# Performance work log

Measured on AMD Instinct MI355X. Metric: run time of the kernel, lower is better.

The kernel has to match this reference:

```python
import jax, jax.numpy as jnp
import numpy as np

V, C, H, L, E, D, B, T = 32000, 1024, 16, 3, 8, 1024, 8, 512
FF = 4 * C
EPS = 1e-5


def setup_inputs() -> dict:
    key = jax.random.key(0)
    ks = iter(jax.random.split(key, 32))
    def w(shape, s=0.02):
        return jax.random.normal(next(ks), shape, jnp.float32) * s
    return {
        "idx": jax.random.randint(next(ks), (B, T), 0, V),
        "tok_emb": w((V, C)),
        "ln1_g": jnp.ones((L, C)), "ln1_b": jnp.zeros((L, C)),
        "ln2_g": jnp.ones((L, C)), "ln2_b": jnp.zeros((L, C)),
        "qkv_w": w((L, C, 3 * C)), "proj_w": w((L, C, C)),
        "ff_w1": w((L, C, FF)), "ff_b1": jnp.zeros((L, FF)),
        "ff_w2": w((L, FF, C)), "ff_b2": jnp.zeros((L, C)),
        "router_w": w((C, E)),
        "exp_w1": w((E, C, D)), "exp_b1": jnp.zeros((E, D)),
        "exp_w2": w((E, D, C)), "exp_b2": jnp.zeros((E, C)),
        "lnf_g": jnp.ones((C,)), "lnf_b": jnp.zeros((C,)),
        "head_w": w((C, V)),
    }


def layernorm(x, g, b):
    m = x.mean(-1, keepdims=True)
    v = x.var(-1, keepdims=True)
    return (x - m) * jax.lax.rsqrt(v + EPS) * g + b


def rope_cos_sin(t, d):
    inv = 1.0 / (10000.0 ** (jnp.arange(0, d, 2, dtype=jnp.float32) / d))
    fr = jnp.arange(t, dtype=jnp.float32)[:, None] * inv[None, :]  # [T, d/2]
    emb = jnp.concatenate([fr, fr], -1)  # [T, d]
    return jnp.cos(emb), jnp.sin(emb)


def rot_half(x):
    x1, x2 = jnp.split(x, 2, axis=-1)
    return jnp.concatenate([-x2, x1], -1)


def attn(x, qkv_w, proj_w):
    b, t, c = x.shape
    d = c // H
    qkv = (x @ qkv_w).reshape(b, t, 3, H, d).transpose(2, 0, 3, 1, 4)  # [3,B,H,T,d]
    q, k, v = qkv[0], qkv[1], qkv[2]
    cos, sin = rope_cos_sin(t, d)
    q = q * cos + rot_half(q) * sin
    k = k * cos + rot_half(k) * sin
    s = jnp.einsum('bhqd,bhkd->bhqk', q, k) / np.float32(np.sqrt(d))
    causal = jnp.tril(jnp.ones((t, t), bool))
    s = jnp.where(causal, s, jnp.float32(-1e30))
    a = jax.nn.softmax(s, -1)
    y = jnp.einsum('bhqk,bhkd->bhqd', a, v)
    y = y.transpose(0, 2, 1, 3).reshape(b, t, c)
    return y @ proj_w


def moe(xf, router_w, exp_w1, exp_b1, exp_w2, exp_b2):
    # router softmax -> top-2 -> renormalize -> scatter into dense [N,E] mask
    probs = jax.nn.softmax(xf @ router_w, -1)
    tw, ti = jax.lax.top_k(probs, 2)
    tw = tw / tw.sum(-1, keepdims=True)
    n = xf.shape[0]
    mask = jnp.zeros((n, E), xf.dtype).at[jnp.arange(n)[:, None], ti].set(tw)
    # per-expert dense FFN over all tokens, combined with sparse weights
    h = jax.nn.gelu(jnp.einsum('nc,ecd->end', xf, exp_w1) + exp_b1[:, None, :], approximate=False)
    y = jnp.einsum('end,edc->enc', h, exp_w2) + exp_b2[:, None, :]
    return jnp.einsum('ne,enc->nc', mask, y)


def reference(idx, tok_emb, ln1_g, ln1_b, ln2_g, ln2_b, qkv_w, proj_w,
              ff_w1, ff_b1, ff_w2, ff_b2, router_w, exp_w1, exp_b1,
              exp_w2, exp_b2, lnf_g, lnf_b, head_w):
    x = tok_emb[idx]  # [B,T,C]
    for l in range(L):
        x = x + attn(layernorm(x, ln1_g[l], ln1_b[l]), qkv_w[l], proj_w[l])
        h = layernorm(x, ln2_g[l], ln2_b[l])
        x = x + (jax.nn.gelu(h @ ff_w1[l] + ff_b1[l], approximate=False) @ ff_w2[l] + ff_b2[l])
    b, t, c = x.shape
    x = moe(x.reshape(b * t, c), router_w, exp_w1, exp_b1, exp_w2, exp_b2).reshape(b, t, c)
    x = layernorm(x, lnf_g, lnf_b)
    return x @ head_w  # logits [B,T,V]
```

## Files before the change

kernel.cpp:

```cpp
#include <hip/hip_runtime.h>
#include <math.h>


#define NTOK  4096
#define CDIM  1024
#define HEADS 16
#define DHEAD 64
#define LAYERS 3
#define NEXP  8
#define DEXP  1024
#define TSEQ  512
#define FFDIM 4096
#define VOCAB 32000
#define C3    3072

typedef __attribute__((ext_vector_type(8))) short short8;
typedef __attribute__((ext_vector_type(4))) float f32x4;

__device__ __forceinline__ unsigned short f2bf(float f) {
  unsigned int u = __builtin_bit_cast(unsigned int, f);
  return (unsigned short)((u + 0x7fffu + ((u >> 16) & 1u)) >> 16);
}
__device__ __forceinline__ float bf2f(unsigned short h) {
  return __builtin_bit_cast(float, ((unsigned int)h) << 16);
}

__global__ __launch_bounds__(256) void embed_kernel(const int* __restrict__ idx,
                                                    const float* __restrict__ emb,
                                                    float* __restrict__ x) {
  int i = blockIdx.x * 256 + threadIdx.x;
  int n = i >> 8, c4 = i & 255;
  const float4* src = (const float4*)(emb + (size_t)idx[n] * CDIM);
  ((float4*)(x + (size_t)n * CDIM))[c4] = src[c4];
}

__global__ void rope_table_kernel(float* __restrict__ ct, float* __restrict__ st) {
  int t = blockIdx.x, p = threadIdx.x;
  float inv = powf(10000.0f, -(float)p / 32.0f);
  float ang = (float)t * inv;
  ct[t * 32 + p] = cosf(ang);
  st[t * 32 + p] = sinf(ang);
}

__global__ __launch_bounds__(256) void qkv_prep_kernel(
    const float* __restrict__ qkv, const float* __restrict__ ct,
    const float* __restrict__ st,
    unsigned short* __restrict__ Qh, unsigned short* __restrict__ Qm,
    unsigned short* __restrict__ Ql,
    unsigned short* __restrict__ Kh, unsigned short* __restrict__ Km,
    unsigned short* __restrict__ Kl,
    unsigned short* __restrict__ Vth, unsigned short* __restrict__ Vtm,
    unsigned short* __restrict__ Vtl) {
  __shared__ unsigned short sVh[64 * 64], sVm[64 * 64], sVl[64 * 64];
  const int tid = threadIdx.x;
  const int tt0 = blockIdx.x * 64, h = blockIdx.y, b = blockIdx.z;
  const int bh = b * HEADS + h;
#pragma unroll
  for (int u = 0; u < 8; u++) {
    int pidx = tid + u * 256;
    int tl = pidx >> 5, p = pidx & 31;
    int t = tt0 + tl;
    size_t nb = ((size_t)(b * TSEQ + t)) * C3 + h * DHEAD;
    float c0 = ct[t * 32 + p], s0 = st[t * 32 + p];
    size_t ob = ((size_t)bh * TSEQ + t) * 64;
    float a = qkv[nb + p], bb = qkv[nb + p + 32];
    float lo = a * c0 - bb * s0, hi = bb * c0 + a * s0;
    unsigned short w0, w1;
    float r;
    w0 = f2bf(lo); r = lo - bf2f(w0); w1 = f2bf(r); r -= bf2f(w1);
    Qh[ob + p] = w0; Qm[ob + p] = w1; Ql[ob + p] = f2bf(r);
    w0 = f2bf(hi); r = hi - bf2f(w0); w1 = f2bf(r); r -= bf2f(w1);
    Qh[ob + p + 32] = w0; Qm[ob + p + 32] = w1; Ql[ob + p + 32] = f2bf(r);
    a = qkv[nb + CDIM + p]; bb = qkv[nb + CDIM + p + 32];
    lo = a * c0 - bb * s0; hi = bb * c0 + a * s0;
    w0 = f2bf(lo); r = lo - bf2f(w0); w1 = f2bf(r); r -= bf2f(w1);
    Kh[ob + p] = w0; Km[ob + p] = w1; Kl[ob + p] = f2bf(r);
    w0 = f2bf(hi); r = hi - bf2f(w0); w1 = f2bf(r); r -= bf2f(w1);
    Kh[ob + p + 32] = w0; Km[ob + p + 32] = w1; Kl[ob + p + 32] = f2bf(r);
  }
#pragma unroll
  for (int u = 0; u < 4; u++) {
    int vidx = tid + u * 256;
    int tl = vidx >> 4, d4 = (vidx & 15) * 4;
    int t = tt0 + tl;
    float4 v = *(const float4*)(qkv + ((size_t)(b * TSEQ + t)) * C3 + 2 * CDIM + h * DHEAD + d4);
    float vv[4] = {v.x, v.y, v.z, v.w};
#pragma unroll
    for (int j = 0; j < 4; j++) {
      unsigned short w0 = f2bf(vv[j]);
      float r = vv[j] - bf2f(w0);
      unsigned short w1 = f2bf(r);
      r -= bf2f(w1);
      sVh[(d4 + j) * 64 + tl] = w0;
      sVm[(d4 + j) * 64 + tl] = w1;
      sVl[(d4 + j) * 64 + tl] = f2bf(r);
    }
  }
  __syncthreads();
#pragma unroll
  for (int u = 0; u < 2; u++) {
    int idx = tid + u * 256;
    int d = idx >> 3, seg = (idx & 7) * 8;
    size_t go = ((size_t)bh * 64 + d) * TSEQ + tt0 + seg;
    *(short8*)(Vth + go) = *(const short8*)(sVh + d * 64 + seg);
    *(short8*)(Vtm + go) = *(const short8*)(sVm + d * 64 + seg);
    *(short8*)(Vtl + go) = *(const short8*)(sVl + d * 64 + seg);
  }
}

__global__ __launch_bounds__(256) void flash_attn_kernel(
    const unsigned short* __restrict__ Qh, const unsigned short* __restrict__ Qm,
    const unsigned short* __restrict__ Ql,
    const unsigned short* __restrict__ Kh, const unsigned short* __restrict__ Km,
    const unsigned short* __restrict__ Kl,
    const unsigned short* __restrict__ Vth, const unsigned short* __restrict__ Vtm,
    const unsigned short* __restrict__ Vtl,
    float* __restrict__ att) {
  __shared__ __align__(16) unsigned short sK[3][2][64 * 32];
  __shared__ __align__(16) unsigned short sV[3][2][64 * 32];
  __shared__ __align__(16) unsigned short sP[3][2][4][16 * 32];
  const int tid = threadIdx.x;
  const int wv = tid >> 6, ln = tid & 63;
  const int qt = blockIdx.x, h = blockIdx.y, b = blockIdx.z;
  const int bh = b * HEADS + h;
  const int lr = ln & 15, lg = ln >> 4;
  const int q0 = qt * 64 + wv * 16;

  const size_t qoff = ((size_t)bh * TSEQ + q0 + lr) * 64 + 8 * lg;
  short8 qf[3][2];
  qf[0][0] = *(const short8*)(Qh + qoff); qf[0][1] = *(const short8*)(Qh + qoff + 32);
  qf[1][0] = *(const short8*)(Qm + qoff); qf[1][1] = *(const short8*)(Qm + qoff + 32);
  qf[2][0] = *(const short8*)(Ql + qoff); qf[2][1] = *(const short8*)(Ql + qoff + 32);

  f32x4 Y[4];
#pragma unroll
  for (int j = 0; j < 4; j++) Y[j] = (f32x4){0.f, 0.f, 0.f, 0.f};
  float m[4] = {-1e30f, -1e30f, -1e30f, -1e30f};
  float l[4] = {0.f, 0.f, 0.f, 0.f};

  const int r0 = tid >> 3, sg = (tid & 7) * 8;
  const int half = sg >> 5, soff = (sg & 31);

  for (int kt = 0; kt <= qt; kt++) {
    const int kb = kt * 64;
    short8 stg[12];
#pragma unroll
    for (int u = 0; u < 2; u++) {
      int row = r0 + 32 * u;
      size_t gk = ((size_t)bh * TSEQ + kb + row) * 64 + sg;
      size_t gv = ((size_t)bh * 64 + row) * TSEQ + kb + sg;
      stg[u * 6 + 0] = *(const short8*)(Kh + gk);
      stg[u * 6 + 1] = *(const short8*)(Km + gk);
      stg[u * 6 + 2] = *(const short8*)(Kl + gk);
      stg[u * 6 + 3] = *(const short8*)(Vth + gv);
      stg[u * 6 + 4] = *(const short8*)(Vtm + gv);
      stg[u * 6 + 5] = *(const short8*)(Vtl + gv);
    }
    __syncthreads();
#pragma unroll
    for (int u = 0; u < 2; u++) {
      int off = (r0 + 32 * u) * 32 + soff;
      *(short8*)(&sK[0][half][off]) = stg[u * 6 + 0];
      *(short8*)(&sK[1][half][off]) = stg[u * 6 + 1];
      *(short8*)(&sK[2][half][off]) = stg[u * 6 + 2];
      *(short8*)(&sV[0][half][off]) = stg[u * 6 + 3];
      *(short8*)(&sV[1][half][off]) = stg[u * 6 + 4];
      *(short8*)(&sV[2][half][off]) = stg[u * 6 + 5];
    }
    __syncthreads();

    f32x4 s[4];
#pragma unroll
    for (int j = 0; j < 4; j++) s[j] = (f32x4){0.f, 0.f, 0.f, 0.f};
#pragma unroll
    for (int j = 0; j < 4; j++) {
      const int ko = (16 * j + lr) * 32 + 8 * lg;
      short8 k0[3], k1[3];
#pragma unroll
      for (int lv = 0; lv < 3; lv++) {
        k0[lv] = *(const short8*)(&sK[lv][0][ko]);
        k1[lv] = *(const short8*)(&sK[lv][1][ko]);
      }
      s[j] = __builtin_amdgcn_mfma_f32_16x16x32_bf16(qf[0][0], k0[0], s[j], 0, 0, 0);
      s[j] = __builtin_amdgcn_mfma_f32_16x16x32_bf16(qf[0][1], k1[0], s[j], 0, 0, 0);
      s[j] = __builtin_amdgcn_mfma_f32_16x16x32_bf16(qf[0][0], k0[1], s[j], 0, 0, 0);
      s[j] = __builtin_amdgcn_mfma_f32_16x16x32_bf16(qf[0][1], k1[1], s[j], 0, 0, 0);
      s[j] = __builtin_amdgcn_mfma_f32_16x16x32_bf16(qf[1][0], k0[0], s[j], 0, 0, 0);
      s[j] = __builtin_amdgcn_mfma_f32_16x16x32_bf16(qf[1][1], k1[0], s[j], 0, 0, 0);
      s[j] = __builtin_amdgcn_mfma_f32_16x16x32_bf16(qf[0][0], k0[2], s[j], 0, 0, 0);
      s[j] = __builtin_amdgcn_mfma_f32_16x16x32_bf16(qf[0][1], k1[2], s[j], 0, 0, 0);
      s[j] = __builtin_amdgcn_mfma_f32_16x16x32_bf16(qf[1][0], k0[1], s[j], 0, 0, 0);
      s[j] = __builtin_amdgcn_mfma_f32_16x16x32_bf16(qf[1][1], k1[1], s[j], 0, 0, 0);
      s[j] = __builtin_amdgcn_mfma_f32_16x16x32_bf16(qf[2][0], k0[0], s[j], 0, 0, 0);
      s[j] = __builtin_amdgcn_mfma_f32_16x16x32_bf16(qf[2][1], k1[0], s[j], 0, 0, 0);
    }

    const bool diag = (kt == qt);
#pragma unroll
    for (int rr = 0; rr < 4; rr++) {
      const int q = q0 + 4 * lg + rr;
      float mx = -1e30f;
#pragma unroll
      for (int j = 0; j < 4; j++) {
        float v = s[j][rr] * 0.125f;
        if (diag && (kb + 16 * j + lr > q)) v = -1e30f;
        s[j][rr] = v;
        mx = fmaxf(mx, v);
      }
      mx = fmaxf(mx, __shfl_xor(mx, 1));
      mx = fmaxf(mx, __shfl_xor(mx, 2));
      mx = fmaxf(mx, __shfl_xor(mx, 4));
      mx = fmaxf(mx, __shfl_xor(mx, 8));
      float mn = fmaxf(m[rr], mx);
      float al = expf(m[rr] - mn);
      m[rr] = mn;
      l[rr] *= al;
#pragma unroll
      for (int j = 0; j < 4; j++) Y[j][rr] *= al;
      float ps = 0.f;
#pragma unroll
      for (int j = 0; j < 4; j++) {
        float p = expf(s[j][rr] - mn);
        s[j][rr] = p;
        ps += p;
      }
      l[rr] += ps;
    }

#pragma unroll
    for (int j = 0; j < 4; j++) {
      const int jh = j >> 1;
      const int col = 16 * (j & 1) + lr;
#pragma unroll
      for (int rr = 0; rr < 4; rr++) {
        float p = s[j][rr];
        unsigned short w0 = f2bf(p);
        float r = p - bf2f(w0);
        unsigned short w1 = f2bf(r);
        r -= bf2f(w1);
        const int o = (4 * lg + rr) * 32 + col;
        sP[0][jh][wv][o] = w0;
        sP[1][jh][wv][o] = w1;
        sP[2][jh][wv][o] = f2bf(r);
      }
    }
    __syncthreads();
    const int po = lr * 32 + 8 * lg;
    short8 pf[3][2];
#pragma unroll
    for (int lv = 0; lv < 3; lv++) {
      pf[lv][0] = *(const short8*)(&sP[lv][0][wv][po]);
      pf[lv][1] = *(const short8*)(&sP[lv][1][wv][po]);
    }
#pragma unroll
    for (int jd = 0; jd < 4; jd++) {
      const int vo = (16 * jd + lr) * 32 + 8 * lg;
      short8 v0[3], v1[3];
#pragma unroll
      for (int lv = 0; lv < 3; lv++) {
        v0[lv] = *(const short8*)(&sV[lv][0][vo]);
        v1[lv] = *(const short8*)(&sV[lv][1][vo]);
      }
      Y[jd] = __builtin_amdgcn_mfma_f32_16x16x32_bf16(pf[0][0], v0[0], Y[jd], 0, 0, 0);
      Y[jd] = __builtin_amdgcn_mfma_f32_16x16x32_bf16(pf[0][1], v1[0], Y[jd], 0, 0, 0);
      Y[jd] = __builtin_amdgcn_mfma_f32_16x16x32_bf16(pf[0][0], v0[1], Y[jd], 0, 0, 0);
      Y[jd] = __builtin_amdgcn_mfma_f32_16x16x32_bf16(pf[0][1], v1[1], Y[jd], 0, 0, 0);
      Y[jd] = __builtin_amdgcn_mfma_f32_16x16x32_bf16(pf[1][0], v0[0], Y[jd], 0, 0, 0);
      Y[jd] = __builtin_amdgcn_mfma_f32_16x16x32_bf16(pf[1][1], v1[0], Y[jd], 0, 0, 0);
      Y[jd] = __builtin_amdgcn_mfma_f32_16x16x32_bf16(pf[0][0], v0[2], Y[jd], 0, 0, 0);
      Y[jd] = __builtin_amdgcn_mfma_f32_16x16x32_bf16(pf[0][1], v1[2], Y[jd], 0, 0, 0);
      Y[jd] = __builtin_amdgcn_mfma_f32_16x16x32_bf16(pf[1][0], v0[1], Y[jd], 0, 0, 0);
      Y[jd] = __builtin_amdgcn_mfma_f32_16x16x32_bf16(pf[1][1], v1[1], Y[jd], 0, 0, 0);
      Y[jd] = __builtin_amdgcn_mfma_f32_16x16x32_bf16(pf[2][0], v0[0], Y[jd], 0, 0, 0);
      Y[jd] = __builtin_amdgcn_mfma_f32_16x16x32_bf16(pf[2][1], v1[0], Y[jd], 0, 0, 0);
    }
  }

#pragma unroll
  for (int rr = 0; rr < 4; rr++) {
    float t = l[rr];
    t += __shfl_xor(t, 1); t += __shfl_xor(t, 2);
    t += __shfl_xor(t, 4); t += __shfl_xor(t, 8);
    l[rr] = 1.0f / t;
  }
#pragma unroll
  for (int jd = 0; jd < 4; jd++) {
    const int d = 16 * jd + lr;
#pragma unroll
    for (int rr = 0; rr < 4; rr++) {
      const int q = q0 + 4 * lg + rr;
      att[((size_t)(b * TSEQ + q)) * CDIM + h * DHEAD + d] = Y[jd][rr] * l[rr];
    }
  }
}

__global__ __launch_bounds__(256) void ln_split_kernel(const float* __restrict__ x,
                                                       unsigned short* __restrict__ yh,
                                                       unsigned short* __restrict__ yl,
                                                       const float* __restrict__ g,
                                                       const float* __restrict__ b) {
  int n = blockIdx.x, tid = threadIdx.x;
  const float4* xr = (const float4*)(x + (size_t)n * CDIM);
  float4 v = xr[tid];
  float s = v.x + v.y + v.z + v.w;
  float ss = v.x * v.x + v.y * v.y + v.z * v.z + v.w * v.w;
  __shared__ float rs[256], rss[256];
  rs[tid] = s; rss[tid] = ss;
  __syncthreads();
  for (int o = 128; o > 0; o >>= 1) {
    if (tid < o) { rs[tid] += rs[tid + o]; rss[tid] += rss[tid + o]; }
    __syncthreads();
  }
  float m = rs[0] * (1.0f / CDIM);
  float var = rss[0] * (1.0f / CDIM) - m * m;
  float r = rsqrtf(var + 1e-5f);
  float4 gv = ((const float4*)g)[tid];
  float4 bv = ((const float4*)b)[tid];
  float o0 = (v.x - m) * r * gv.x + bv.x;
  float o1 = (v.y - m) * r * gv.y + bv.y;
  float o2 = (v.z - m) * r * gv.z + bv.z;
  float o3 = (v.w - m) * r * gv.w + bv.w;
  ushort4 hh, ll;
  hh.x = f2bf(o0); ll.x = f2bf(o0 - bf2f(hh.x));
  hh.y = f2bf(o1); ll.y = f2bf(o1 - bf2f(hh.y));
  hh.z = f2bf(o2); ll.z = f2bf(o2 - bf2f(hh.z));
  hh.w = f2bf(o3); ll.w = f2bf(o3 - bf2f(hh.w));
  ((ushort4*)(yh + (size_t)n * CDIM))[tid] = hh;
  ((ushort4*)(yl + (size_t)n * CDIM))[tid] = ll;
}

__global__ __launch_bounds__(256) void cvt_split_kernel(const float* __restrict__ x,
                                                        unsigned short* __restrict__ yh,
                                                        unsigned short* __restrict__ yl) {
  int i = blockIdx.x * 256 + threadIdx.x;
  float4 v = ((const float4*)x)[i];
  ushort4 hh, ll;
  hh.x = f2bf(v.x); ll.x = f2bf(v.x - bf2f(hh.x));
  hh.y = f2bf(v.y); ll.y = f2bf(v.y - bf2f(hh.y));
  hh.z = f2bf(v.z); ll.z = f2bf(v.z - bf2f(hh.z));
  hh.w = f2bf(v.w); ll.w = f2bf(v.w - bf2f(hh.w));
  ((ushort4*)yh)[i] = hh;
  ((ushort4*)yl)[i] = ll;
}

__global__ __launch_bounds__(256) void cvt_bf16_kernel(const float* __restrict__ x,
                                                       unsigned short* __restrict__ y) {
  int i = blockIdx.x * 256 + threadIdx.x;
  float4 v = ((const float4*)x)[i];
  ushort4 o;
  o.x = f2bf(v.x); o.y = f2bf(v.y); o.z = f2bf(v.z); o.w = f2bf(v.w);
  ((ushort4*)y)[i] = o;
}

__global__ __launch_bounds__(256) void ln_bf16_kernel(const float* __restrict__ x,
                                                      unsigned short* __restrict__ y,
                                                      const float* __restrict__ g,
                                                      const float* __restrict__ b) {
  int n = blockIdx.x, tid = threadIdx.x;
  const float4* xr = (const float4*)(x + (size_t)n * CDIM);
  float4 v = xr[tid];
  float s = v.x + v.y + v.z + v.w;
  float ss = v.x * v.x + v.y * v.y + v.z * v.z + v.w * v.w;
  __shared__ float rs[256], rss[256];
  rs[tid] = s; rss[tid] = ss;
  __syncthreads();
  for (int o = 128; o > 0; o >>= 1) {
    if (tid < o) { rs[tid] += rs[tid + o]; rss[tid] += rss[tid + o]; }
    __syncthreads();
  }
  float m = rs[0] * (1.0f / CDIM);
  float var = rss[0] * (1.0f / CDIM) - m * m;
  float r = rsqrtf(var + 1e-5f);
  float4 gv = ((const float4*)g)[tid];
  float4 bv = ((const float4*)b)[tid];
  ushort4 o4;
  o4.x = f2bf((v.x - m) * r * gv.x + bv.x);
  o4.y = f2bf((v.y - m) * r * gv.y + bv.y);
  o4.z = f2bf((v.z - m) * r * gv.z + bv.z);
  o4.w = f2bf((v.w - m) * r * gv.w + bv.w);
  ((ushort4*)(y + (size_t)n * CDIM))[tid] = o4;
}

__global__ __launch_bounds__(256) void biasgelu_cvt_kernel(const float* __restrict__ in,
                                                           const float* __restrict__ bias,
                                                           unsigned short* __restrict__ out,
                                                           int Fm4) {
  int i = blockIdx.x * 256 + threadIdx.x;
  int c4 = (i & (Fm4 - 1)) << 2;
  float4 v = ((const float4*)in)[i];
  float4 b = *(const float4*)(bias + c4);
  float a0 = v.x + b.x, a1 = v.y + b.y, a2 = v.z + b.z, a3 = v.w + b.w;
  ushort4 o;
  o.x = f2bf(0.5f * a0 * (1.0f + erff(a0 * 0.70710678118654752f)));
  o.y = f2bf(0.5f * a1 * (1.0f + erff(a1 * 0.70710678118654752f)));
  o.z = f2bf(0.5f * a2 * (1.0f + erff(a2 * 0.70710678118654752f)));
  o.w = f2bf(0.5f * a3 * (1.0f + erff(a3 * 0.70710678118654752f)));
  ((ushort4*)out)[i] = o;
}

__global__ __launch_bounds__(256) void addres_kernel(float* __restrict__ x,
                                                     const float* __restrict__ t) {
  int i = blockIdx.x * 256 + threadIdx.x;
  float4 xv = ((const float4*)x)[i];
  float4 tv = ((const float4*)t)[i];
  xv.x += tv.x; xv.y += tv.y; xv.z += tv.z; xv.w += tv.w;
  ((float4*)x)[i] = xv;
}

__global__ __launch_bounds__(256) void add2_kernel(float* __restrict__ x,
                                                   const float* __restrict__ t,
                                                   const float* __restrict__ bias) {
  int i = blockIdx.x * 256 + threadIdx.x;
  int c4 = (i & (CDIM / 4 - 1)) << 2;
  float4 xv = ((const float4*)x)[i];
  float4 tv = ((const float4*)t)[i];
  float4 b = *(const float4*)(bias + c4);
  xv.x += tv.x + b.x; xv.y += tv.y + b.y; xv.z += tv.z + b.z; xv.w += tv.w + b.w;
  ((float4*)x)[i] = xv;
}

__global__ __launch_bounds__(256) void scaleadd_kernel(float* __restrict__ o,
                                                       const float* __restrict__ t,
                                                       const float* __restrict__ bias,
                                                       const float* __restrict__ rs) {
  int i = blockIdx.x * 256 + threadIdx.x;
  int m = i >> 8;
  int c4 = (i & (CDIM / 4 - 1)) << 2;
  float w = rs[m];
  float4 ov = ((const float4*)o)[i];
  float4 tv = ((const float4*)t)[i];
  float4 b = *(const float4*)(bias + c4);
  ov.x += w * (tv.x + b.x); ov.y += w * (tv.y + b.y);
  ov.z += w * (tv.z + b.z); ov.w += w * (tv.w + b.w);
  ((float4*)o)[i] = ov;
}

__global__ __launch_bounds__(256) void wconv_t_kernel(const float* __restrict__ W,
                                                      unsigned short* __restrict__ Wt,
                                                      int K, int N) {
  __shared__ float t[32][33];
  int n0 = blockIdx.x * 32, k0 = blockIdx.y * 32;
  int tx = threadIdx.x & 31, ty = threadIdx.x >> 5;
#pragma unroll
  for (int i = 0; i < 4; i++)
    t[ty + 8 * i][tx] = W[(size_t)(k0 + ty + 8 * i) * N + n0 + tx];
  __syncthreads();
#pragma unroll
  for (int i = 0; i < 4; i++)
    Wt[(size_t)(n0 + ty + 8 * i) * K + k0 + tx] = f2bf(t[tx][ty + 8 * i]);
}

__global__ __launch_bounds__(256) void wconv_split_kernel(const float* __restrict__ W,
                                                          unsigned short* __restrict__ Wh,
                                                          unsigned short* __restrict__ Wl,
                                                          int K, int N) {
  __shared__ float t[32][33];
  int n0 = blockIdx.x * 32, k0 = blockIdx.y * 32;
  int tx = threadIdx.x & 31, ty = threadIdx.x >> 5;
#pragma unroll
  for (int i = 0; i < 4; i++)
    t[ty + 8 * i][tx] = W[(size_t)(k0 + ty + 8 * i) * N + n0 + tx];
  __syncthreads();
#pragma unroll
  for (int i = 0; i < 4; i++) {
    float w = t[tx][ty + 8 * i];
    unsigned short h = f2bf(w);
    size_t o = (size_t)(n0 + ty + 8 * i) * K + k0 + tx;
    Wh[o] = h;
    Wl[o] = f2bf(w - bf2f(h));
  }
}

template <int FUSE>
__global__ __launch_bounds__(256) void gemm_split(const unsigned short* __restrict__ Ah,
                                                  const unsigned short* __restrict__ Al,
                                                  const unsigned short* __restrict__ Bth,
                                                  const unsigned short* __restrict__ Btl,
                                                  float* __restrict__ C,
                                                  unsigned short* __restrict__ Ch,
                                                  unsigned short* __restrict__ Cl,
                                                  const float* __restrict__ bias,
                                                  int M, int Nn, int K) {
  __shared__ __align__(16) unsigned short AsH[128 * 32];
  __shared__ __align__(16) unsigned short AsL[128 * 32];
  __shared__ __align__(16) unsigned short BsH[128 * 32];
  __shared__ __align__(16) unsigned short BsL[128 * 32];
  const int tid = threadIdx.x;
  const int wv = tid >> 6, ln = tid & 63;
  const int bm = blockIdx.y * 128, bn = blockIdx.x * 128;

  const size_t aoff0 = (size_t)(bm + 32 * wv + (ln >> 2)) * K + (size_t)((ln & 3) * 8);
  const size_t aoff1 = aoff0 + (size_t)16 * K;
  const size_t boff0 = (size_t)(bn + 32 * wv + (ln >> 2)) * K + (size_t)((ln & 3) * 8);
  const size_t boff1 = boff0 + (size_t)16 * K;
  const int lofs = 1024 * wv + ln * 8;

  const int wm = wv >> 1, wn = wv & 1;
  const int lr = ln & 15, lg = ln >> 4;

  f32x4 acc[4][4];
#pragma unroll
  for (int i = 0; i < 4; i++)
#pragma unroll
    for (int j = 0; j < 4; j++) acc[i][j] = (f32x4){0.f, 0.f, 0.f, 0.f};

  for (int k0 = 0; k0 < K; k0 += 32) {
    short8 rah0 = *(const short8*)(Ah + aoff0 + k0);
    short8 rah1 = *(const short8*)(Ah + aoff1 + k0);
    short8 ral0 = *(const short8*)(Al + aoff0 + k0);
    short8 ral1 = *(const short8*)(Al + aoff1 + k0);
    short8 rbh0 = *(const short8*)(Bth + boff0 + k0);
    short8 rbh1 = *(const short8*)(Bth + boff1 + k0);
    short8 rbl0 = *(const short8*)(Btl + boff0 + k0);
    short8 rbl1 = *(const short8*)(Btl + boff1 + k0);
    __syncthreads();
    *(short8*)(AsH + lofs)       = rah0;
    *(short8*)(AsH + lofs + 512) = rah1;
    *(short8*)(AsL + lofs)       = ral0;
    *(short8*)(AsL + lofs + 512) = ral1;
    *(short8*)(BsH + lofs)       = rbh0;
    *(short8*)(BsH + lofs + 512) = rbh1;
    *(short8*)(BsL + lofs)       = rbl0;
    *(short8*)(BsL + lofs + 512) = rbl1;
    __syncthreads();

    short8 afh[4], afl[4], bwh[4], bwl[4];
#pragma unroll
    for (int i = 0; i < 4; i++) {
      const int ao = (64 * wm + 16 * i + lr) * 32 + 8 * lg;
      afh[i] = *(const short8*)(AsH + ao);
      afl[i] = *(const short8*)(AsL + ao);
    }
#pragma unroll
    for (int j = 0; j < 4; j++) {
      const int bo = (64 * wn + 16 * j + lr) * 32 + 8 * lg;
      bwh[j] = *(const short8*)(BsH + bo);
      bwl[j] = *(const short8*)(BsL + bo);
    }
#pragma unroll
    for (int i = 0; i < 4; i++)
#pragma unroll
      for (int j = 0; j < 4; j++) {
        acc[i][j] = __builtin_amdgcn_mfma_f32_16x16x32_bf16(afh[i], bwh[j], acc[i][j], 0, 0, 0);
        acc[i][j] = __builtin_amdgcn_mfma_f32_16x16x32_bf16(afl[i], bwh[j], acc[i][j], 0, 0, 0);
        acc[i][j] = __builtin_amdgcn_mfma_f32_16x16x32_bf16(afh[i], bwl[j], acc[i][j], 0, 0, 0);
      }
  }

#pragma unroll
  for (int j = 0; j < 4; j++) {
    const int n = bn + 64 * wn + 16 * j + lr;
#pragma unroll
    for (int i = 0; i < 4; i++) {
#pragma unroll
      for (int rr = 0; rr < 4; rr++) {
        const int m = bm + 64 * wm + 16 * i + 4 * lg + rr;
        float v = acc[i][j][rr];
        const size_t ci = (size_t)m * Nn + n;
        if constexpr (FUSE == 1) {
          v += bias[n];
          v = 0.5f * v * (1.0f + erff(v * 0.70710678118654752f));
          unsigned short h = f2bf(v);
          Ch[ci] = h;
          Cl[ci] = f2bf(v - bf2f(h));
        } else {
          C[ci] = v;
        }
      }
    }
  }
}

__global__ __launch_bounds__(256) void gemm_bf16(const unsigned short* __restrict__ A,
                                                 const unsigned short* __restrict__ Bt,
                                                 float* __restrict__ C,
                                                 int M, int Nn, int K) {
  __shared__ __align__(16) unsigned short As[128 * 32];
  __shared__ __align__(16) unsigned short Bs[128 * 32];
  const int tid = threadIdx.x;
  const int wv = tid >> 6, ln = tid & 63;
  const int bm = blockIdx.y * 128, bn = blockIdx.x * 128;

  const size_t aoff0 = (size_t)(bm + 32 * wv + (ln >> 2)) * K + (size_t)((ln & 3) * 8);
  const size_t aoff1 = aoff0 + (size_t)16 * K;
  const size_t boff0 = (size_t)(bn + 32 * wv + (ln >> 2)) * K + (size_t)((ln & 3) * 8);
  const size_t boff1 = boff0 + (size_t)16 * K;
  const int lofs = 1024 * wv + ln * 8;

  const int wm = wv >> 1, wn = wv & 1;
  const int lr = ln & 15, lg = ln >> 4;

  f32x4 acc[4][4];
#pragma unroll
  for (int i = 0; i < 4; i++)
#pragma unroll
    for (int j = 0; j < 4; j++) acc[i][j] = (f32x4){0.f, 0.f, 0.f, 0.f};

  for (int k0 = 0; k0 < K; k0 += 32) {
    short8 ra0 = *(const short8*)(A + aoff0 + k0);
    short8 ra1 = *(const short8*)(A + aoff1 + k0);
    short8 rb0 = *(const short8*)(Bt + boff0 + k0);
    short8 rb1 = *(const short8*)(Bt + boff1 + k0);
    __syncthreads();
    *(short8*)(As + lofs)       = ra0;
    *(short8*)(As + lofs + 512) = ra1;
    *(short8*)(Bs + lofs)       = rb0;
    *(short8*)(Bs + lofs + 512) = rb1;
    __syncthreads();

    short8 af[4], bw[4];
#pragma unroll
    for (int i = 0; i < 4; i++)
      af[i] = *(const short8*)(As + ((64 * wm + 16 * i + lr) * 32 + 8 * lg));
#pragma unroll
    for (int j = 0; j < 4; j++)
      bw[j] = *(const short8*)(Bs + ((64 * wn + 16 * j + lr) * 32 + 8 * lg));
#pragma unroll
    for (int i = 0; i < 4; i++)
#pragma unroll
      for (int j = 0; j < 4; j++)
        acc[i][j] = __builtin_amdgcn_mfma_f32_16x16x32_bf16(af[i], bw[j], acc[i][j], 0, 0, 0);
  }

#pragma unroll
  for (int j = 0; j < 4; j++) {
    const int n = bn + 64 * wn + 16 * j + lr;
#pragma unroll
    for (int i = 0; i < 4; i++) {
#pragma unroll
      for (int r = 0; r < 4; r++) {
        const int m = bm + 64 * wm + 16 * i + 4 * lg + r;
        C[(size_t)m * Nn + n] = acc[i][j][r];
      }
    }
  }
}

__global__ __launch_bounds__(64) void router_kernel(const float* __restrict__ x,
                                                    const float* __restrict__ rw,
                                                    float* __restrict__ maskT) {
  int n = blockIdx.x, lane = threadIdx.x;
  const float* xr = x + (size_t)n * CDIM;
  float acc[NEXP] = {};
  for (int i = 0; i < CDIM / 64; i++) {
    int c = lane + 64 * i;
    float xv = xr[c];
    const float* r = rw + (size_t)c * NEXP;
#pragma unroll
    for (int e = 0; e < NEXP; e++) acc[e] += xv * r[e];
  }
  for (int m = 32; m >= 1; m >>= 1)
#pragma unroll
    for (int e = 0; e < NEXP; e++) acc[e] += __shfl_xor(acc[e], m);
  if (lane == 0) {
    float mx = acc[0];
#pragma unroll
    for (int e = 1; e < NEXP; e++) mx = fmaxf(mx, acc[e]);
    float p[NEXP];
#pragma unroll
    for (int e = 0; e < NEXP; e++) p[e] = expf(acc[e] - mx);
    int i1 = 0;
#pragma unroll
    for (int e = 1; e < NEXP; e++) if (p[e] > p[i1]) i1 = e;
    int i2 = (i1 == 0) ? 1 : 0;
#pragma unroll
    for (int e = 0; e < NEXP; e++) if (e != i1 && p[e] > p[i2]) i2 = e;
    float denom = p[i1] + p[i2];
    float w1 = p[i1] / denom, w2 = p[i2] / denom;
#pragma unroll
    for (int e = 0; e < NEXP; e++) maskT[(size_t)e * NTOK + n] = 0.0f;
    maskT[(size_t)i1 * NTOK + n] = w1;
    maskT[(size_t)i2 * NTOK + n] = w2;
  }
}

extern "C" void kernel_launch(void* const* d_in, const int* in_sizes, int n_in,
                              void* d_out, int out_size, void* d_ws, size_t ws_size,
                              hipStream_t stream) {
  const int*   idx      = (const int*)d_in[0];
  const float* tok_emb  = (const float*)d_in[1];
  const float* ln1_g    = (const float*)d_in[2];
  const float* ln1_b    = (const float*)d_in[3];
  const float* ln2_g    = (const float*)d_in[4];
  const float* ln2_b    = (const float*)d_in[5];
  const float* qkv_w    = (const float*)d_in[6];
  const float* proj_w   = (const float*)d_in[7];
  const float* ff_w1    = (const float*)d_in[8];
  const float* ff_b1    = (const float*)d_in[9];
  const float* ff_w2    = (const float*)d_in[10];
  const float* ff_b2    = (const float*)d_in[11];
  const float* router_w = (const float*)d_in[12];
  const float* exp_w1   = (const float*)d_in[13];
  const float* exp_b1   = (const float*)d_in[14];
  const float* exp_w2   = (const float*)d_in[15];
  const float* exp_b2   = (const float*)d_in[16];
  const float* lnf_g    = (const float*)d_in[17];
  const float* lnf_b    = (const float*)d_in[18];
  const float* head_w   = (const float*)d_in[19];
  float* out = (float*)d_out;

  const size_t NC = (size_t)NTOK * CDIM;
  char* w = (char*)d_ws;
  float* x  = (float*)w;                 w += NC * 4;
  unsigned short* S1 = (unsigned short*)w; w += NC * 4;
  float* Q  = (float*)w;                 w += (size_t)NTOK * C3 * 4;
  float* C3r = (float*)w;                w += NC * 4;
  unsigned short* WS = (unsigned short*)w; w += NC * 4;
  unsigned short* EX = (unsigned short*)w; w += NC * 6;
  float* maskT = (float*)w;              w += (size_t)NEXP * NTOK * 4;
  float* ct = (float*)w;                 w += (size_t)TSEQ * 32 * 4;
  float* st = (float*)w;                 w += (size_t)TSEQ * 32 * 4;

  unsigned short* xh = S1;
  unsigned short* xl = S1 + NC;
  unsigned short* Wh = WS;
  unsigned short* Wl = WS + NC;
  float* qkvf = Q;
  unsigned short* Qh_s = S1;
  unsigned short* Qm_s = S1 + NC;
  unsigned short* Ql_s = EX;
  unsigned short* Kh_s = (unsigned short*)C3r;
  unsigned short* Km_s = (unsigned short*)C3r + NC;
  unsigned short* Kl_s = EX + NC;
  unsigned short* Vth_s = WS;
  unsigned short* Vtm_s = WS + NC;
  unsigned short* Vtl_s = EX + 2 * NC;
  float* att_f = Q;
  unsigned short* hh = (unsigned short*)Q;
  unsigned short* hl = (unsigned short*)Q + (size_t)NTOK * FFDIM;
  float* tmpS1 = (float*)S1;
  float* projf = C3r;
  unsigned short* x_bf    = S1;
  unsigned short* hmoe_bf = S1 + NC;
  float* hmoe_f32 = C3r;
  float* tmp2     = Q;
  float* moe_out  = x;
  unsigned short* wt_s = WS;
  unsigned short* xn_bf   = S1;
  unsigned short* wt_head = (unsigned short*)Q;

  embed_kernel<<<NTOK, 256, 0, stream>>>(idx, tok_emb, x);
  rope_table_kernel<<<TSEQ, 32, 0, stream>>>(ct, st);

  for (int l = 0; l < LAYERS; l++) {
    ln_split_kernel<<<NTOK, 256, 0, stream>>>(x, xh, xl, ln1_g + l * CDIM, ln1_b + l * CDIM);
    wconv_split_kernel<<<dim3(C3 / 32, CDIM / 32), 256, 0, stream>>>(
        qkv_w + (size_t)l * CDIM * C3, Wh, Wl, CDIM, C3);
    gemm_split<0><<<dim3(C3 / 128, NTOK / 128), 256, 0, stream>>>(
        xh, xl, Wh, Wl, qkvf, nullptr, nullptr, nullptr, NTOK, C3, CDIM);
    qkv_prep_kernel<<<dim3(TSEQ / 64, HEADS, 8), 256, 0, stream>>>(
        qkvf, ct, st, Qh_s, Qm_s, Ql_s, Kh_s, Km_s, Kl_s, Vth_s, Vtm_s, Vtl_s);
    flash_attn_kernel<<<dim3(TSEQ / 64, HEADS, 8), 256, 0, stream>>>(
        Qh_s, Qm_s, Ql_s, Kh_s, Km_s, Kl_s, Vth_s, Vtm_s, Vtl_s, att_f);
    cvt_split_kernel<<<(NC / 4) / 256, 256, 0, stream>>>(att_f, xh, xl);
    wconv_split_kernel<<<dim3(CDIM / 32, CDIM / 32), 256, 0, stream>>>(
        proj_w + (size_t)l * CDIM * CDIM, Wh, Wl, CDIM, CDIM);
    gemm_split<0><<<dim3(CDIM / 128, NTOK / 128), 256, 0, stream>>>(
        xh, xl, Wh, Wl, projf, nullptr, nullptr, nullptr, NTOK, CDIM, CDIM);
    addres_kernel<<<(NC / 4) / 256, 256, 0, stream>>>(x, projf);
    ln_split_kernel<<<NTOK, 256, 0, stream>>>(x, xh, xl, ln2_g + l * CDIM, ln2_b + l * CDIM);
    wconv_split_kernel<<<dim3(FFDIM / 32, CDIM / 32), 256, 0, stream>>>(
        ff_w1 + (size_t)l * CDIM * FFDIM, Wh, Wl, CDIM, FFDIM);
    gemm_split<1><<<dim3(FFDIM / 128, NTOK / 128), 256, 0, stream>>>(
        xh, xl, Wh, Wl, nullptr, hh, hl, ff_b1 + (size_t)l * FFDIM, NTOK, FFDIM, CDIM);
    wconv_split_kernel<<<dim3(CDIM / 32, FFDIM / 32), 256, 0, stream>>>(
        ff_w2 + (size_t)l * FFDIM * CDIM, Wh, Wl, FFDIM, CDIM);
    gemm_split<0><<<dim3(CDIM / 128, NTOK / 128), 256, 0, stream>>>(
        hh, hl, Wh, Wl, tmpS1, nullptr, nullptr, nullptr, NTOK, CDIM, FFDIM);
    add2_kernel<<<(NC / 4) / 256, 256, 0, stream>>>(x, tmpS1, ff_b2 + (size_t)l * CDIM);
  }

  router_kernel<<<NTOK, 64, 0, stream>>>(x, router_w, maskT);
  cvt_bf16_kernel<<<(NC / 4) / 256, 256, 0, stream>>>(x, x_bf);
  hipMemsetAsync(moe_out, 0, NC * sizeof(float), stream);
  for (int e = 0; e < NEXP; e++) {
    wconv_t_kernel<<<dim3(DEXP / 32, CDIM / 32), 256, 0, stream>>>(
        exp_w1 + (size_t)e * CDIM * DEXP, wt_s, CDIM, DEXP);
    gemm_bf16<<<dim3(DEXP / 128, NTOK / 128), 256, 0, stream>>>(
        x_bf, wt_s, hmoe_f32, NTOK, DEXP, CDIM);
    biasgelu_cvt_kernel<<<((int)(NC / 4)) / 256, 256, 0, stream>>>(
        hmoe_f32, exp_b1 + (size_t)e * DEXP, hmoe_bf, DEXP / 4);
    wconv_t_kernel<<<dim3(CDIM / 32, DEXP / 32), 256, 0, stream>>>(
        exp_w2 + (size_t)e * DEXP * CDIM, wt_s, DEXP, CDIM);
    gemm_bf16<<<dim3(CDIM / 128, NTOK / 128), 256, 0, stream>>>(
        hmoe_bf, wt_s, tmp2, NTOK, CDIM, DEXP);
    scaleadd_kernel<<<((int)(NC / 4)) / 256, 256, 0, stream>>>(
        moe_out, tmp2, exp_b2 + (size_t)e * CDIM, maskT + (size_t)e * NTOK);
  }

  ln_bf16_kernel<<<NTOK, 256, 0, stream>>>(moe_out, xn_bf, lnf_g, lnf_b);
  wconv_t_kernel<<<dim3(VOCAB / 32, CDIM / 32), 256, 0, stream>>>(head_w, wt_head, CDIM, VOCAB);
  gemm_bf16<<<dim3(VOCAB / 128, NTOK / 128), 256, 0, stream>>>(
      xn_bf, wt_head, out, NTOK, VOCAB, CDIM);
}
```

Baseline: 2.960 ms.

## Fuse elementwise epilogues into GEMMs and attention, add XCD-aware block swizzle

Several standalone elementwise kernels are folded into the kernels that produce their inputs. Residual add, bias-add, GELU with bf16 conversion, and router-weighted expert accumulation now run in GEMM epilogues through MODE templates, and flash attention writes the hi/lo bf16 split directly. This removes several full fp32 round-trips through global memory per layer and per expert, plus the associated launches. GEMM block indices are also remapped so that neighbouring tiles are grouped onto the same XCD, aiming for better L2 reuse. The trade-off is read-modify-write epilogues with scalar strided stores, and somewhat higher register use in the GEMMs.

```diff
diff --git a/kernel.cpp b/kernel.cpp
--- a/kernel.cpp
+++ b/kernel.cpp
@@ -115,7 +115,7 @@
     const unsigned short* __restrict__ Kl,
     const unsigned short* __restrict__ Vth, const unsigned short* __restrict__ Vtm,
     const unsigned short* __restrict__ Vtl,
-    float* __restrict__ att) {
+    unsigned short* __restrict__ ath, unsigned short* __restrict__ atl) {
   __shared__ __align__(16) unsigned short sK[3][2][64 * 32];
   __shared__ __align__(16) unsigned short sV[3][2][64 * 32];
   __shared__ __align__(16) unsigned short sP[3][2][4][16 * 32];
@@ -289,7 +289,11 @@
 #pragma unroll
     for (int rr = 0; rr < 4; rr++) {
       const int q = q0 + 4 * lg + rr;
-      att[((size_t)(b * TSEQ + q)) * CDIM + h * DHEAD + d] = Y[jd][rr] * l[rr];
+      float v = Y[jd][rr] * l[rr];
+      unsigned short w0 = f2bf(v);
+      const size_t ci = ((size_t)(b * TSEQ + q)) * CDIM + h * DHEAD + d;
+      ath[ci] = w0;
+      atl[ci] = f2bf(v - bf2f(w0));
     }
   }
 }
@@ -329,20 +333,6 @@
   ((ushort4*)(yl + (size_t)n * CDIM))[tid] = ll;
 }
 
-__global__ __launch_bounds__(256) void cvt_split_kernel(const float* __restrict__ x,
-                                                        unsigned short* __restrict__ yh,
-                                                        unsigned short* __restrict__ yl) {
-  int i = blockIdx.x * 256 + threadIdx.x;
-  float4 v = ((const float4*)x)[i];
-  ushort4 hh, ll;
-  hh.x = f2bf(v.x); ll.x = f2bf(v.x - bf2f(hh.x));
-  hh.y = f2bf(v.y); ll.y = f2bf(v.y - bf2f(hh.y));
-  hh.z = f2bf(v.z); ll.z = f2bf(v.z - bf2f(hh.z));
-  hh.w = f2bf(v.w); ll.w = f2bf(v.w - bf2f(hh.w));
-  ((ushort4*)yh)[i] = hh;
-  ((ushort4*)yl)[i] = ll;
-}
-
 __global__ __launch_bounds__(256) void cvt_bf16_kernel(const float* __restrict__ x,
                                                        unsigned short* __restrict__ y) {
   int i = blockIdx.x * 256 + threadIdx.x;
@@ -381,60 +371,6 @@
   ((ushort4*)(y + (size_t)n * CDIM))[tid] = o4;
 }
 
-__global__ __launch_bounds__(256) void biasgelu_cvt_kernel(const float* __restrict__ in,
-                                                           const float* __restrict__ bias,
-                                                           unsigned short* __restrict__ out,
-                                                           int Fm4) {
-  int i = blockIdx.x * 256 + threadIdx.x;
-  int c4 = (i & (Fm4 - 1)) << 2;
-  float4 v = ((const float4*)in)[i];
-  float4 b = *(const float4*)(bias + c4);
-  float a0 = v.x + b.x, a1 = v.y + b.y, a2 = v.z + b.z, a3 = v.w + b.w;
-  ushort4 o;
-  o.x = f2bf(0.5f * a0 * (1.0f + erff(a0 * 0.70710678118654752f)));
-  o.y = f2bf(0.5f * a1 * (1.0f + erff(a1 * 0.70710678118654752f)));
-  o.z = f2bf(0.5f * a2 * (1.0f + erff(a2 * 0.70710678118654752f)));
-  o.w = f2bf(0.5f * a3 * (1.0f + erff(a3 * 0.70710678118654752f)));
-  ((ushort4*)out)[i] = o;
-}
-
-__global__ __launch_bounds__(256) void addres_kernel(float* __restrict__ x,
-                                                     const float* __restrict__ t) {
-  int i = blockIdx.x * 256 + threadIdx.x;
-  float4 xv = ((const float4*)x)[i];
-  float4 tv = ((const float4*)t)[i];
-  xv.x += tv.x; xv.y += tv.y; xv.z += tv.z; xv.w += tv.w;
-  ((float4*)x)[i] = xv;
-}
-
-__global__ __launch_bounds__(256) void add2_kernel(float* __restrict__ x,
-                                                   const float* __restrict__ t,
-                                                   const float* __restrict__ bias) {
-  int i = blockIdx.x * 256 + threadIdx.x;
-  int c4 = (i & (CDIM / 4 - 1)) << 2;
-  float4 xv = ((const float4*)x)[i];
-  float4 tv = ((const float4*)t)[i];
-  float4 b = *(const float4*)(bias + c4);
-  xv.x += tv.x + b.x; xv.y += tv.y + b.y; xv.z += tv.z + b.z; xv.w += tv.w + b.w;
-  ((float4*)x)[i] = xv;
-}
-
-__global__ __launch_bounds__(256) void scaleadd_kernel(float* __restrict__ o,
-                                                       const float* __restrict__ t,
-                                                       const float* __restrict__ bias,
-                                                       const float* __restrict__ rs) {
-  int i = blockIdx.x * 256 + threadIdx.x;
-  int m = i >> 8;
-  int c4 = (i & (CDIM / 4 - 1)) << 2;
-  float w = rs[m];
-  float4 ov = ((const float4*)o)[i];
-  float4 tv = ((const float4*)t)[i];
-  float4 b = *(const float4*)(bias + c4);
-  ov.x += w * (tv.x + b.x); ov.y += w * (tv.y + b.y);
-  ov.z += w * (tv.z + b.z); ov.w += w * (tv.w + b.w);
-  ((float4*)o)[i] = ov;
-}
-
 __global__ __launch_bounds__(256) void wconv_t_kernel(const float* __restrict__ W,
                                                       unsigned short* __restrict__ Wt,
                                                       int K, int N) {
@@ -471,7 +407,15 @@
   }
 }
 
-template <int FUSE>
+__device__ __forceinline__ void xcd_swz(int& bx, int& by) {
+  int bid = blockIdx.y * gridDim.x + blockIdx.x;
+  int cpx = (gridDim.x * gridDim.y) >> 3;
+  bid = (bid & 7) * cpx + (bid >> 3);
+  bx = bid % gridDim.x;
+  by = bid / gridDim.x;
+}
+
+template <int MODE>
 __global__ __launch_bounds__(256) void gemm_split(const unsigned short* __restrict__ Ah,
                                                   const unsigned short* __restrict__ Al,
                                                   const unsigned short* __restrict__ Bth,
@@ -487,7 +431,9 @@
   __shared__ __align__(16) unsigned short BsL[128 * 32];
   const int tid = threadIdx.x;
   const int wv = tid >> 6, ln = tid & 63;
-  const int bm = blockIdx.y * 128, bn = blockIdx.x * 128;
+  int sbx, sby;
+  xcd_swz(sbx, sby);
+  const int bm = sby * 128, bn = sbx * 128;
 
   const size_t aoff0 = (size_t)(bm + 32 * wv + (ln >> 2)) * K + (size_t)((ln & 3) * 8);
   const size_t aoff1 = aoff0 + (size_t)16 * K;
@@ -550,6 +496,7 @@
 #pragma unroll
   for (int j = 0; j < 4; j++) {
     const int n = bn + 64 * wn + 16 * j + lr;
+    const float bb = (MODE == 1 || MODE == 3) ? bias[n] : 0.0f;
 #pragma unroll
     for (int i = 0; i < 4; i++) {
 #pragma unroll
@@ -557,29 +504,39 @@
         const int m = bm + 64 * wm + 16 * i + 4 * lg + rr;
         float v = acc[i][j][rr];
         const size_t ci = (size_t)m * Nn + n;
-        if constexpr (FUSE == 1) {
-          v += bias[n];
+        if constexpr (MODE == 0) {
+          C[ci] = v;
+        } else if constexpr (MODE == 1) {
+          v += bb;
           v = 0.5f * v * (1.0f + erff(v * 0.70710678118654752f));
           unsigned short h = f2bf(v);
           Ch[ci] = h;
           Cl[ci] = f2bf(v - bf2f(h));
+        } else if constexpr (MODE == 2) {
+          C[ci] += v;
         } else {
-          C[ci] = v;
+          C[ci] += v + bb;
         }
       }
     }
   }
 }
 
+template <int MODE>
 __global__ __launch_bounds__(256) void gemm_bf16(const unsigned short* __restrict__ A,
                                                  const unsigned short* __restrict__ Bt,
                                                  float* __restrict__ C,
+                                                 unsigned short* __restrict__ Cu,
+                                                 const float* __restrict__ bias,
+                                                 const float* __restrict__ rowscale,
                                                  int M, int Nn, int K) {
   __shared__ __align__(16) unsigned short As[128 * 32];
   __shared__ __align__(16) unsigned short Bs[128 * 32];
   const int tid = threadIdx.x;
   const int wv = tid >> 6, ln = tid & 63;
-  const int bm = blockIdx.y * 128, bn = blockIdx.x * 128;
+  int sbx, sby;
+  xcd_swz(sbx, sby);
+  const int bm = sby * 128, bn = sbx * 128;
 
   const size_t aoff0 = (size_t)(bm + 32 * wv + (ln >> 2)) * K + (size_t)((ln & 3) * 8);
   const size_t aoff1 = aoff0 + (size_t)16 * K;
@@ -625,12 +582,23 @@
 #pragma unroll
   for (int j = 0; j < 4; j++) {
     const int n = bn + 64 * wn + 16 * j + lr;
+    const float bb = (MODE != 0) ? bias[n] : 0.0f;
 #pragma unroll
     for (int i = 0; i < 4; i++) {
 #pragma unroll
       for (int r = 0; r < 4; r++) {
         const int m = bm + 64 * wm + 16 * i + 4 * lg + r;
-        C[(size_t)m * Nn + n] = acc[i][j][r];
+        float v = acc[i][j][r];
+        const size_t ci = (size_t)m * Nn + n;
+        if constexpr (MODE == 0) {
+          C[ci] = v;
+        } else if constexpr (MODE == 1) {
+          v += bb;
+          v = 0.5f * v * (1.0f + erff(v * 0.70710678118654752f));
+          Cu[ci] = f2bf(v);
+        } else {
+          C[ci] += rowscale[m] * (v + bb);
+        }
       }
     }
   }
@@ -725,15 +693,12 @@
   unsigned short* Vth_s = WS;
   unsigned short* Vtm_s = WS + NC;
   unsigned short* Vtl_s = EX + 2 * NC;
-  float* att_f = Q;
+  unsigned short* ath = (unsigned short*)Q;
+  unsigned short* atl = (unsigned short*)Q + NC;
   unsigned short* hh = (unsigned short*)Q;
   unsigned short* hl = (unsigned short*)Q + (size_t)NTOK * FFDIM;
-  float* tmpS1 = (float*)S1;
-  float* projf = C3r;
   unsigned short* x_bf    = S1;
   unsigned short* hmoe_bf = S1 + NC;
-  float* hmoe_f32 = C3r;
-  float* tmp2     = Q;
   float* moe_out  = x;
   unsigned short* wt_s = WS;
   unsigned short* xn_bf   = S1;
@@ -751,13 +716,11 @@
     qkv_prep_kernel<<<dim3(TSEQ / 64, HEADS, 8), 256, 0, stream>>>(
         qkvf, ct, st, Qh_s, Qm_s, Ql_s, Kh_s, Km_s, Kl_s, Vth_s, Vtm_s, Vtl_s);
     flash_attn_kernel<<<dim3(TSEQ / 64, HEADS, 8), 256, 0, stream>>>(
-        Qh_s, Qm_s, Ql_s, Kh_s, Km_s, Kl_s, Vth_s, Vtm_s, Vtl_s, att_f);
-    cvt_split_kernel<<<(NC / 4) / 256, 256, 0, stream>>>(att_f, xh, xl);
+        Qh_s, Qm_s, Ql_s, Kh_s, Km_s, Kl_s, Vth_s, Vtm_s, Vtl_s, ath, atl);
     wconv_split_kernel<<<dim3(CDIM / 32, CDIM / 32), 256, 0, stream>>>(
         proj_w + (size_t)l * CDIM * CDIM, Wh, Wl, CDIM, CDIM);
-    gemm_split<0><<<dim3(CDIM / 128, NTOK / 128), 256, 0, stream>>>(
-        xh, xl, Wh, Wl, projf, nullptr, nullptr, nullptr, NTOK, CDIM, CDIM);
-    addres_kernel<<<(NC / 4) / 256, 256, 0, stream>>>(x, projf);
+    gemm_split<2><<<dim3(CDIM / 128, NTOK / 128), 256, 0, stream>>>(
+        ath, atl, Wh, Wl, x, nullptr, nullptr, nullptr, NTOK, CDIM, CDIM);
     ln_split_kernel<<<NTOK, 256, 0, stream>>>(x, xh, xl, ln2_g + l * CDIM, ln2_b + l * CDIM);
     wconv_split_kernel<<<dim3(FFDIM / 32, CDIM / 32), 256, 0, stream>>>(
         ff_w1 + (size_t)l * CDIM * FFDIM, Wh, Wl, CDIM, FFDIM);
@@ -765,9 +728,8 @@
         xh, xl, Wh, Wl, nullptr, hh, hl, ff_b1 + (size_t)l * FFDIM, NTOK, FFDIM, CDIM);
     wconv_split_kernel<<<dim3(CDIM / 32, FFDIM / 32), 256, 0, stream>>>(
         ff_w2 + (size_t)l * FFDIM * CDIM, Wh, Wl, FFDIM, CDIM);
-    gemm_split<0><<<dim3(CDIM / 128, NTOK / 128), 256, 0, stream>>>(
-        hh, hl, Wh, Wl, tmpS1, nullptr, nullptr, nullptr, NTOK, CDIM, FFDIM);
-    add2_kernel<<<(NC / 4) / 256, 256, 0, stream>>>(x, tmpS1, ff_b2 + (size_t)l * CDIM);
+    gemm_split<3><<<dim3(CDIM / 128, NTOK / 128), 256, 0, stream>>>(
+        hh, hl, Wh, Wl, x, nullptr, nullptr, ff_b2 + (size_t)l * CDIM, NTOK, CDIM, FFDIM);
   }
 
   router_kernel<<<NTOK, 64, 0, stream>>>(x, router_w, maskT);
@@ -776,20 +738,17 @@
   for (int e = 0; e < NEXP; e++) {
     wconv_t_kernel<<<dim3(DEXP / 32, CDIM / 32), 256, 0, stream>>>(
         exp_w1 + (size_t)e * CDIM * DEXP, wt_s, CDIM, DEXP);
-    gemm_bf16<<<dim3(DEXP / 128, NTOK / 128), 256, 0, stream>>>(
-        x_bf, wt_s, hmoe_f32, NTOK, DEXP, CDIM);
-    biasgelu_cvt_kernel<<<((int)(NC / 4)) / 256, 256, 0, stream>>>(
-        hmoe_f32, exp_b1 + (size_t)e * DEXP, hmoe_bf, DEXP / 4);
+    gemm_bf16<1><<<dim3(DEXP / 128, NTOK / 128), 256, 0, stream>>>(
+        x_bf, wt_s, nullptr, hmoe_bf, exp_b1 + (size_t)e * DEXP, nullptr, NTOK, DEXP, CDIM);
     wconv_t_kernel<<<dim3(CDIM / 32, DEXP / 32), 256, 0, stream>>>(
         exp_w2 + (size_t)e * DEXP * CDIM, wt_s, DEXP, CDIM);
-    gemm_bf16<<<dim3(CDIM / 128, NTOK / 128), 256, 0, stream>>>(
-        hmoe_bf, wt_s, tmp2, NTOK, CDIM, DEXP);
-    scaleadd_kernel<<<((int)(NC / 4)) / 256, 256, 0, stream>>>(
-        moe_out, tmp2, exp_b2 + (size_t)e * CDIM, maskT + (size_t)e * NTOK);
+    gemm_bf16<2><<<dim3(CDIM / 128, NTOK / 128), 256, 0, stream>>>(
+        hmoe_bf, wt_s, moe_out, nullptr, exp_b2 + (size_t)e * CDIM,
+        maskT + (size_t)e * NTOK, NTOK, CDIM, DEXP);
   }
 
   ln_bf16_kernel<<<NTOK, 256, 0, stream>>>(moe_out, xn_bf, lnf_g, lnf_b);
   wconv_t_kernel<<<dim3(VOCAB / 32, CDIM / 32), 256, 0, stream>>>(head_w, wt_head, CDIM, VOCAB);
-  gemm_bf16<<<dim3(VOCAB / 128, NTOK / 128), 256, 0, stream>>>(
-      xn_bf, wt_head, out, NTOK, VOCAB, CDIM);
-}
+  gemm_bf16<0><<<dim3(VOCAB / 128, NTOK / 128), 256, 0, stream>>>(
+      xn_bf, wt_head, out, nullptr, nullptr, nullptr, NTOK, VOCAB, CDIM);
+}
```

After: 2.865 ms. -3.2%, faster.
